# Kernel optimization log

Measured on AMD Instinct MI355X. Metric: run time of the kernel, lower is better.

The kernel has to match this reference:

```python
import jax, jax.numpy as jnp
import numpy as np

N_HEADS = 4
DIM_K = 64
DIM_V = 64
D_MODEL = 256


def setup_inputs() -> dict:
    key = jax.random.key(0)
    ks = jax.random.split(key, 10)
    B, S = 8, 1024
    s = 1.0 / np.sqrt(D_MODEL)
    return {
        "x": jax.random.normal(ks[0], (B, S, D_MODEL), jnp.float32),
        "y": jax.random.normal(ks[1], (B, S, D_MODEL), jnp.float32),
        "Wq": jax.random.normal(ks[2], (D_MODEL, DIM_K * N_HEADS), jnp.float32) * s,
        "bq": jnp.zeros((DIM_K * N_HEADS,), jnp.float32),
        "Wk": jax.random.normal(ks[3], (D_MODEL, DIM_K * N_HEADS), jnp.float32) * s,
        "bk": jnp.zeros((DIM_K * N_HEADS,), jnp.float32),
        "Wv": jax.random.normal(ks[4], (D_MODEL, DIM_V * N_HEADS), jnp.float32) * s,
        "bv": jnp.zeros((DIM_V * N_HEADS,), jnp.float32),
        "Wo": jax.random.normal(ks[5], (DIM_V * N_HEADS, D_MODEL), jnp.float32) * s,
        "bo": jnp.zeros((D_MODEL,), jnp.float32),
    }


def reference(x, y, Wq, bq, Wk, bk, Wv, bv, Wo, bo):
    B, Sx, _ = x.shape
    Sy = y.shape[1]
    dk = DIM_K // N_HEADS  # head dim for Q/K (16)
    dv = DIM_V // N_HEADS  # head dim for V (16)
    # Faithful to the original reshape: leading dim becomes n_heads^2 pseudo-heads.
    Q = (x @ Wq + bq).reshape(-1, B, Sx, dk)   # [H2, B, Sx, dk]
    K = (y @ Wk + bk).reshape(-1, B, Sy, dk)   # [H2, B, Sy, dk]
    V = (y @ Wv + bv).reshape(-1, B, Sy, dv)   # [H2, B, Sy, dv]
    scale = 1.0 / np.sqrt(DIM_K)
    scores = jnp.einsum("hbqd,hbkd->hbqk", Q, K) * scale  # [H2, B, Sx, Sy]
    # Per-row lower median (torch.median semantics: lower of two middle values).
    n = scores.shape[-1]
    med = jnp.sort(scores, axis=-1)[..., (n - 1) // 2][..., None]
    # Mask out entries not strictly greater than the row median.
    scores = jnp.where(scores - med > 0, scores, -jnp.inf)
    probs = jax.nn.softmax(scores, axis=-1)
    out = jnp.einsum("hbqk,hbkd->hbqd", probs, V)          # [H2, B, Sx, dv]
    out = jnp.transpose(out, (0, 2, 1, 3)).reshape(B, Sx, -1)  # [B, Sx, H2*dv]
    return out @ Wo + bo
```

## Files before the change

### kernel.cpp

```cpp
#include <hip/hip_runtime.h>
#include <stdint.h>


typedef _Float16 f16x8 __attribute__((ext_vector_type(8)));
typedef _Float16 f16x4 __attribute__((ext_vector_type(4)));
typedef float    f32x4 __attribute__((ext_vector_type(4)));

__global__ __launch_bounds__(256) void prepW(
    const float* __restrict__ Wq, const float* __restrict__ Wk,
    const float* __restrict__ Wv, const float* __restrict__ Wo,
    _Float16* __restrict__ P)
{
    __shared__ float T[64][65];
    const int mat = blockIdx.y;
    const float* W = (mat == 0) ? Wq : (mat == 1) ? Wk : (mat == 2) ? Wv : Wo;
    const int tk = blockIdx.x >> 2, tn = blockIdx.x & 3;
    const int t  = threadIdx.x;
    const int cl = t & 63, rg = t >> 6;

    #pragma unroll
    for (int r = 0; r < 16; ++r) {
        const int k = (rg << 4) + r;
        T[k][cl] = W[(size_t)((tk << 6) + k) * 256 + (tn << 6) + cl];
    }
    __syncthreads();
    _Float16* hi = P + ((size_t)mat << 17);
    _Float16* lo = hi + 65536;
    #pragma unroll
    for (int r = 0; r < 16; ++r) {
        const int n = (rg << 4) + r;
        const float v = T[cl][n];
        const _Float16 h = (_Float16)v;
        const size_t o = (size_t)((tn << 6) + n) * 256 + (tk << 6) + cl;
        hi[o] = h;
        lo[o] = (_Float16)(v - (float)h);
    }
}

__device__ __forceinline__ void gemm_mfma(const float* __restrict__ A,
                                          const _Float16* __restrict__ Whi,
                                          const _Float16* __restrict__ Wlo,
                                          const float* __restrict__ bias,
                                          float* __restrict__ C, int vf16)
{
    __shared__ _Float16 Bhi[64][136];
    __shared__ _Float16 Blo[64][136];
    const int tid = threadIdx.x;
    const int m0 = blockIdx.x << 7, n0 = blockIdx.y << 6;

    const int wv = tid >> 6, lane = tid & 63;
    const int fm = lane & 15, fq = lane >> 4;
    const int arow = m0 + (wv << 4) + fm;
    const float* abase = A + (size_t)arow * 256;

    const int srow = tid >> 4;
    const int skl  = (tid & 15) << 3;

    f32x4 acc[4];
    #pragma unroll
    for (int cb = 0; cb < 4; ++cb) { acc[cb][0]=0.f; acc[cb][1]=0.f; acc[cb][2]=0.f; acc[cb][3]=0.f; }

    float4 a0 = *(const float4*)(abase + (fq << 3));
    float4 a1 = *(const float4*)(abase + (fq << 3) + 4);

    #pragma unroll
    for (int h = 0; h < 2; ++h) {
        if (h) __syncthreads();
        #pragma unroll
        for (int p = 0; p < 2; ++p) {
            const int n = (p << 5) + srow;
            const size_t off = (size_t)(n0 + n) * 256 + (h << 7) + skl;
            *(f16x8*)&Bhi[n][skl] = *(const f16x8*)(Whi + off);
            *(f16x8*)&Blo[n][skl] = *(const f16x8*)(Wlo + off);
        }
        __syncthreads();

        #pragma unroll
        for (int kb = 0; kb < 4; ++kb) {
            const int ks = (h << 2) + kb;
            float4 n0v = a0, n1v = a1;
            if (ks < 7) {
                const float* np = abase + ((ks + 1) << 5) + (fq << 3);
                n0v = *(const float4*)np;
                n1v = *(const float4*)(np + 4);
            }
            const float ae[8] = {a0.x, a0.y, a0.z, a0.w, a1.x, a1.y, a1.z, a1.w};
            f16x8 Ah, Al;
            #pragma unroll
            for (int j = 0; j < 8; ++j) {
                const _Float16 hh = (_Float16)ae[j];
                Ah[j] = hh;
                Al[j] = (_Float16)(ae[j] - (float)hh);
            }
            #pragma unroll
            for (int cb = 0; cb < 4; ++cb) {
                f16x8 Bh = *(const f16x8*)&Bhi[(cb << 4) + fm][(kb << 5) + (fq << 3)];
                f16x8 Bl = *(const f16x8*)&Blo[(cb << 4) + fm][(kb << 5) + (fq << 3)];
                acc[cb] = __builtin_amdgcn_mfma_f32_16x16x32_f16(Ah, Bh, acc[cb], 0, 0, 0);
                acc[cb] = __builtin_amdgcn_mfma_f32_16x16x32_f16(Al, Bh, acc[cb], 0, 0, 0);
                acc[cb] = __builtin_amdgcn_mfma_f32_16x16x32_f16(Ah, Bl, acc[cb], 0, 0, 0);
            }
            a0 = n0v; a1 = n1v;
        }
    }

    if (vf16) {
        _Float16* Vt = (_Float16*)C;
        float bb[4];
        #pragma unroll
        for (int cb = 0; cb < 4; ++cb) bb[cb] = bias[n0 + (cb << 4) + fm];
        #pragma unroll
        for (int i = 0; i < 4; ++i) {
            const int m = m0 + (wv << 4) + (fq << 2) + i;
            f16x4 v;
            #pragma unroll
            for (int cb = 0; cb < 4; ++cb)
                v[cb] = (_Float16)(acc[cb][i] + bb[cb]);
            const size_t o = ((size_t)(m >> 6) << 14) + ((size_t)fm << 10)
                           + ((m & 63) << 4) + (n0 >> 4);
            *(f16x4*)&Vt[o] = v;
        }
    } else {
        #pragma unroll
        for (int cb = 0; cb < 4; ++cb) {
            const float bb = bias[n0 + (cb << 4) + fm];
            #pragma unroll
            for (int i = 0; i < 4; ++i)
                C[(size_t)(m0 + (wv << 4) + (fq << 2) + i) * 256
                  + n0 + (cb << 4) + fm] = acc[cb][i] + bb;
        }
    }
}

__global__ __attribute__((amdgpu_waves_per_eu(6, 6)))
__launch_bounds__(512) void gemmQKV(
    const float* __restrict__ x, const float* __restrict__ y,
    const _Float16* __restrict__ WP,
    const float* __restrict__ bq, const float* __restrict__ bk,
    const float* __restrict__ bv,
    float* __restrict__ Q, float* __restrict__ K, float* __restrict__ Vf)
{
    const int z = blockIdx.z;
    const float* A = (z == 0) ? x  : y;
    const _Float16* Whi = WP + ((size_t)z << 17);
    const _Float16* Wlo = Whi + 65536;
    const float* b = (z == 0) ? bq : (z == 1) ? bk : bv;
    float*       C = (z == 0) ? Q  : (z == 1) ? K  : Vf;
    gemm_mfma(A, Whi, Wlo, b, C, z == 2);
}

__global__ __attribute__((amdgpu_waves_per_eu(6, 6)))
__launch_bounds__(512) void gemmOut(
    const float* __restrict__ A, const _Float16* __restrict__ WP,
    const float* __restrict__ b, float* __restrict__ C)
{
    const _Float16* Whi = WP + ((size_t)3 << 17);
    const _Float16* Wlo = Whi + 65536;
    gemm_mfma(A, Whi, Wlo, b, C, 0);
}

__device__ __forceinline__ float u2f(unsigned int m) {
    unsigned int x = (m & 0x80000000u) ? (m ^ 0x80000000u) : ~m;
    return __uint_as_float(x);
}
__device__ __forceinline__ unsigned int f2u(float f) {
    unsigned int x = __float_as_uint(f);
    return (x & 0x80000000u) ? ~x : (x | 0x80000000u);
}

__device__ __forceinline__ float wred_sum(float x) {
    x += __int_as_float(__builtin_amdgcn_update_dpp(0, __float_as_int(x), 0x111, 0xF, 0xF, true));
    x += __int_as_float(__builtin_amdgcn_update_dpp(0, __float_as_int(x), 0x112, 0xF, 0xF, true));
    x += __int_as_float(__builtin_amdgcn_update_dpp(0, __float_as_int(x), 0x114, 0xF, 0xF, true));
    x += __int_as_float(__builtin_amdgcn_update_dpp(0, __float_as_int(x), 0x118, 0xF, 0xF, true));
    x += __int_as_float(__builtin_amdgcn_update_dpp(0, __float_as_int(x), 0x142, 0xF, 0xF, true));
    x += __int_as_float(__builtin_amdgcn_update_dpp(0, __float_as_int(x), 0x143, 0xF, 0xF, true));
    return __int_as_float(__builtin_amdgcn_readlane(__float_as_int(x), 63));
}
__device__ __forceinline__ float wred_min(float x) {
    const int IDENT = 0x7f7fffff;
    x = fminf(x, __int_as_float(__builtin_amdgcn_update_dpp(IDENT, __float_as_int(x), 0x111, 0xF, 0xF, false)));
    x = fminf(x, __int_as_float(__builtin_amdgcn_update_dpp(IDENT, __float_as_int(x), 0x112, 0xF, 0xF, false)));
    x = fminf(x, __int_as_float(__builtin_amdgcn_update_dpp(IDENT, __float_as_int(x), 0x114, 0xF, 0xF, false)));
    x = fminf(x, __int_as_float(__builtin_amdgcn_update_dpp(IDENT, __float_as_int(x), 0x118, 0xF, 0xF, false)));
    x = fminf(x, __int_as_float(__builtin_amdgcn_update_dpp(IDENT, __float_as_int(x), 0x142, 0xF, 0xF, false)));
    x = fminf(x, __int_as_float(__builtin_amdgcn_update_dpp(IDENT, __float_as_int(x), 0x143, 0xF, 0xF, false)));
    return __int_as_float(__builtin_amdgcn_readlane(__float_as_int(x), 63));
}
__device__ __forceinline__ float wred_max(float x) {
    const int IDENT = (int)0xff7fffff;
    x = fmaxf(x, __int_as_float(__builtin_amdgcn_update_dpp(IDENT, __float_as_int(x), 0x111, 0xF, 0xF, false)));
    x = fmaxf(x, __int_as_float(__builtin_amdgcn_update_dpp(IDENT, __float_as_int(x), 0x112, 0xF, 0xF, false)));
    x = fmaxf(x, __int_as_float(__builtin_amdgcn_update_dpp(IDENT, __float_as_int(x), 0x114, 0xF, 0xF, false)));
    x = fmaxf(x, __int_as_float(__builtin_amdgcn_update_dpp(IDENT, __float_as_int(x), 0x118, 0xF, 0xF, false)));
    x = fmaxf(x, __int_as_float(__builtin_amdgcn_update_dpp(IDENT, __float_as_int(x), 0x142, 0xF, 0xF, false)));
    x = fmaxf(x, __int_as_float(__builtin_amdgcn_update_dpp(IDENT, __float_as_int(x), 0x143, 0xF, 0xF, false)));
    return __int_as_float(__builtin_amdgcn_readlane(__float_as_int(x), 63));
}

__global__ __attribute__((amdgpu_waves_per_eu(6, 6)))
__launch_bounds__(512) void attn(
    const float* __restrict__ Qb, const float* __restrict__ Kb,
    const _Float16* __restrict__ Vb, float* __restrict__ Ob)
{
    __shared__ float Ssc[8][1028];
    __shared__ float part[1024];
    __shared__ float sums[2][8];

    const int tid  = threadIdx.x;
    const int wave = tid >> 6, lane = tid & 63;
    const int head = blockIdx.x, grp = blockIdx.y;
    const float*    Qh = Qb + ((size_t)head << 14);
    const float*    Kh = Kb + ((size_t)head << 14);
    const _Float16* Vh = Vb + ((size_t)head << 14);
    const int fm = lane & 15, fq = lane >> 4;

    f16x8 Bp[8];
    #pragma unroll
    for (int kb = 0; kb < 8; ++kb) {
        const int krow = (wave << 7) + (kb << 4) + fm;
        float4 kv = *(const float4*)(Kh + ((size_t)krow << 4) + (fq << 2));
        const float ke[4] = {kv.x * 0.125f, kv.y * 0.125f,
                             kv.z * 0.125f, kv.w * 0.125f};
        #pragma unroll
        for (int j = 0; j < 4; ++j) {
            _Float16 h = (_Float16)ke[j];
            Bp[kb][j]     = h;
            Bp[kb][j + 4] = (_Float16)(ke[j] - (float)h);
        }
    }
    const _Float16* vfb = Vh + ((size_t)fm << 10) + (wave << 7) + (fq << 3);

    const int cstart = (grp * 128) / 6;
    const int cend   = ((grp + 1) * 128) / 6;

    for (int chunk = cstart; chunk < cend; ++chunk) {
        const int qbase = chunk << 3;
        const int sb = chunk & 1;

        f16x8 A1, A2;
        {
            const int arow = qbase + (fm & 7);
            float4 qv = *(const float4*)(Qh + ((size_t)arow << 4) + (fq << 2));
            const float qe[4] = {qv.x, qv.y, qv.z, qv.w};
            #pragma unroll
            for (int j = 0; j < 4; ++j) {
                _Float16 h = (_Float16)qe[j];
                A1[j] = h; A1[j + 4] = h;
                A2[j] = (_Float16)(qe[j] - (float)h);
                A2[j + 4] = (_Float16)0.f;
            }
        }
        #pragma unroll
        for (int kb = 0; kb < 8; ++kb) {
            f32x4 c = {0.f, 0.f, 0.f, 0.f};
            c = __builtin_amdgcn_mfma_f32_16x16x32_f16(A1, Bp[kb], c, 0, 0, 0);
            c = __builtin_amdgcn_mfma_f32_16x16x32_f16(A2, Bp[kb], c, 0, 0, 0);
            if (fq < 2) {
                const int col = (wave << 7) + (kb << 4) + fm;
                #pragma unroll
                for (int i = 0; i < 4; ++i)
                    Ssc[(fq << 2) + i][col] = c[i];
            }
        }
        __syncthreads();

        float s[16];
        #pragma unroll
        for (int b = 0; b < 4; ++b) {
            f32x4 v = *(const f32x4*)&Ssc[wave][(b << 8) + (lane << 2)];
            s[(b << 2) + 0] = v.x; s[(b << 2) + 1] = v.y;
            s[(b << 2) + 2] = v.z; s[(b << 2) + 3] = v.w;
        }

        float mn = 0.f, sq = 0.f;
        #pragma unroll
        for (int j = 0; j < 16; ++j) { mn += s[j]; sq += s[j] * s[j]; }
        mn = wred_sum(mn);
        sq = wred_sum(sq);
        mn *= (1.0f / 1024.0f);
        const float var  = fmaxf(sq * (1.0f / 1024.0f) - mn * mn, 1e-12f);
        const float step = __builtin_sqrtf(var) * 0.0024479f;

        unsigned int lo = 0x00800000u, hi = 0xFF7FFFFFu;
        int cl = 0, ch = 1024;
        float vL = -3.4e38f, vH = 3.4e38f;
        float t = mn, medf = 0.f;
        int found = 0;
        for (int pass = 0; pass < 64 && !found; ++pass) {
            int cnt = 0;
            #pragma unroll
            for (int j = 0; j < 16; ++j)
                cnt += __popcll(__ballot(s[j] <= t));
            const unsigned int tc = f2u(t);
            if (cnt >= 512) { hi = tc; ch = cnt; vH = t; }
            else            { lo = tc + 1; cl = cnt; vL = t; }

            if (cl == 511) {
                float c = 3.4e38f;
                #pragma unroll
                for (int j = 0; j < 16; ++j)
                    c = fminf(c, (s[j] > vL) ? s[j] : 3.4e38f);
                medf = wred_min(c); found = 1;
            } else if (ch == 512) {
                float c = -3.4e38f;
                #pragma unroll
                for (int j = 0; j < 16; ++j)
                    c = fmaxf(c, (s[j] <= vH) ? s[j] : -3.4e38f);
                medf = wred_max(c); found = 1;
            } else if (cl == 510) {
                float m1 = 3.4e38f;
                #pragma unroll
                for (int j = 0; j < 16; ++j)
                    m1 = fminf(m1, (s[j] > vL) ? s[j] : 3.4e38f);
                m1 = wred_min(m1);
                int c1 = 0;
                #pragma unroll
                for (int j = 0; j < 16; ++j)
                    c1 += __popcll(__ballot(s[j] <= m1));
                if (c1 >= 512) { medf = m1; }
                else {
                    float c2 = 3.4e38f;
                    #pragma unroll
                    for (int j = 0; j < 16; ++j)
                        c2 = fminf(c2, (s[j] > m1) ? s[j] : 3.4e38f);
                    medf = wred_min(c2);
                }
                found = 1;
            } else if (ch == 513) {
                float m1 = -3.4e38f;
                #pragma unroll
                for (int j = 0; j < 16; ++j)
                    m1 = fmaxf(m1, (s[j] <= vH) ? s[j] : -3.4e38f);
                m1 = wred_max(m1);
                int c1 = 0;
                #pragma unroll
                for (int j = 0; j < 16; ++j)
                    c1 += __popcll(__ballot(s[j] < m1));
                if (c1 <= 511) { medf = m1; }
                else {
                    float c2 = -3.4e38f;
                    #pragma unroll
                    for (int j = 0; j < 16; ++j)
                        c2 = fmaxf(c2, (s[j] < m1) ? s[j] : -3.4e38f);
                    medf = wred_max(c2);
                }
                found = 1;
            } else if (lo >= hi) {
                medf = u2f(lo); found = 1;
            } else {
                float tn = t + (511.5f - (float)cnt) * step;
                bool ok = (tn > vL) && (tn < vH);
                if (pass >= 5 && (pass & 1)) ok = false;
                t = ok ? tn : u2f(lo + ((hi - lo) >> 1));
            }
        }
        if (!found) medf = u2f(lo);

        _Float16* Pw = (_Float16*)&Ssc[wave][0];
        float sum = 0.f;
        #pragma unroll
        for (int b = 0; b < 4; ++b) {
            f16x4 hv;
            #pragma unroll
            for (int jj = 0; jj < 4; ++jj) {
                float e = (s[(b << 2) + jj] > medf) ? __expf(s[(b << 2) + jj]) : 0.f;
                _Float16 h = (_Float16)e;
                hv[jj] = h;
                sum += (float)h;
            }
            *(f16x4*)&Pw[(b << 8) + (lane << 2)] = hv;
        }
        sum = wred_sum(sum);
        if (lane == 0) sums[sb][wave] = sum;
        __syncthreads();

        f32x4 acc = {0.f, 0.f, 0.f, 0.f};
        const _Float16* Pr = (const _Float16*)&Ssc[fm & 7][0] + (fq << 3);
        #pragma unroll
        for (int kb = 0; kb < 4; ++kb) {
            f16x8 vf = *(const f16x8*)(vfb + (kb << 5));
            f16x8 a = *(const f16x8*)(Pr + ((((wave << 2) + kb)) << 5));
            acc = __builtin_amdgcn_mfma_f32_16x16x32_f16(a, vf, acc, 0, 0, 0);
        }
        if (lane < 32) {
            #pragma unroll
            for (int i = 0; i < 4; ++i)
                part[(wave << 7) + (((fq << 2) + i) << 4) + fm] = acc[i];
        }
        __syncthreads();

        const int rw = (wave - chunk) & 7;
        if (rw < 2) {
            const int t2 = (rw << 6) + lane;
            const int r = t2 >> 4, d = t2 & 15;
            float o = 0.f;
            #pragma unroll
            for (int w = 0; w < 8; ++w) o += part[(w << 7) + t2];
            const float inv = 1.0f / sums[sb][r];
            const int q = qbase + r;
            const int h = head >> 3, bp = head & 7;
            float* dst = Ob + (((size_t)(h >> 1)) << 18)
                            + ((size_t)(((h & 1) << 9) + (q >> 1)) << 8)
                            + ((q & 1) << 7) + (bp << 4) + d;
            *dst = o * inv;
        }
    }
}

extern "C" void kernel_launch(void* const* d_in, const int* in_sizes, int n_in,
                              void* d_out, int out_size, void* d_ws, size_t ws_size,
                              hipStream_t stream) {
    const float* x  = (const float*)d_in[0];
    const float* y  = (const float*)d_in[1];
    const float* Wq = (const float*)d_in[2];
    const float* bq = (const float*)d_in[3];
    const float* Wk = (const float*)d_in[4];
    const float* bk = (const float*)d_in[5];
    const float* Wv = (const float*)d_in[6];
    const float* bv = (const float*)d_in[7];
    const float* Wo = (const float*)d_in[8];
    const float* bo = (const float*)d_in[9];
    float* out = (float*)d_out;

    float*     Q  = (float*)d_ws;
    float*     K  = Q + 2097152;
    _Float16*  VT = (_Float16*)(K + 2097152);
    float*     AO = (float*)d_ws + 5242880;
    _Float16*  WP = (_Float16*)((float*)d_ws + 7340032);

    prepW<<<dim3(16, 4), dim3(256), 0, stream>>>(Wq, Wk, Wv, Wo, WP);
    gemmQKV<<<dim3(64, 4, 3), dim3(512), 0, stream>>>(x, y, WP, bq, bk, bv,
                                                      Q, K, (float*)VT);
    attn<<<dim3(128, 6), dim3(512), 0, stream>>>(Q, K, VT, AO);
    gemmOut<<<dim3(64, 4), dim3(512), 0, stream>>>(AO, WP, bo, out);
}
```

Measured before the change: 260.4 us.

## Pre-swizzle weights into MFMA fragment layout and read directly from global

prepW now writes the hi/lo fp16 weight split in the exact per-lane MFMA B-fragment order, so the GEMM kernels load B fragments straight from global memory with 16-byte loads. This removes the LDS staging and both __syncthreads in the GEMM. Blocks shrink to 256 threads covering 64 rows, and the grids double to keep the same coverage. The cost is redundant B reads from global/L2 across blocks and one fewer wave of latency hiding per block.

```diff
diff --git a/kernel.cpp b/kernel.cpp
--- a/kernel.cpp
+++ b/kernel.cpp
@@ -27,13 +27,23 @@
     _Float16* hi = P + ((size_t)mat << 17);
     _Float16* lo = hi + 65536;
     #pragma unroll
-    for (int r = 0; r < 16; ++r) {
-        const int n = (rg << 4) + r;
-        const float v = T[cl][n];
-        const _Float16 h = (_Float16)v;
-        const size_t o = (size_t)((tn << 6) + n) * 256 + (tk << 6) + cl;
-        hi[o] = h;
-        lo[o] = (_Float16)(v - (float)h);
+    for (int ff = 0; ff < 2; ++ff) {
+        const int f    = (ff << 8) + t;
+        const int lane = f & 63, cb = (f >> 6) & 3, kbl = f >> 8;
+        const int fm = lane & 15, fq = lane >> 4;
+        const int kb = (tk << 1) + kbl;
+        const size_t dst = ((size_t)tn << 14) + ((size_t)((kb << 2) + cb) << 9)
+                         + ((size_t)lane << 3);
+        f16x8 vh, vl;
+        #pragma unroll
+        for (int j = 0; j < 8; ++j) {
+            const float v = T[(kbl << 5) + (fq << 3) + j][(cb << 4) + fm];
+            const _Float16 h = (_Float16)v;
+            vh[j] = h;
+            vl[j] = (_Float16)(v - (float)h);
+        }
+        *(f16x8*)&hi[dst] = vh;
+        *(f16x8*)&lo[dst] = vl;
     }
 }
 
@@ -43,18 +53,15 @@
                                           const float* __restrict__ bias,
                                           float* __restrict__ C, int vf16)
 {
-    __shared__ _Float16 Bhi[64][136];
-    __shared__ _Float16 Blo[64][136];
     const int tid = threadIdx.x;
-    const int m0 = blockIdx.x << 7, n0 = blockIdx.y << 6;
+    const int m0 = blockIdx.x << 6, n0 = blockIdx.y << 6;
 
     const int wv = tid >> 6, lane = tid & 63;
     const int fm = lane & 15, fq = lane >> 4;
     const int arow = m0 + (wv << 4) + fm;
     const float* abase = A + (size_t)arow * 256;
-
-    const int srow = tid >> 4;
-    const int skl  = (tid & 15) << 3;
+    const _Float16* bhF = Whi + ((size_t)blockIdx.y << 14) + ((size_t)lane << 3);
+    const _Float16* blF = Wlo + ((size_t)blockIdx.y << 14) + ((size_t)lane << 3);
 
     f32x4 acc[4];
     #pragma unroll
@@ -64,44 +71,31 @@
     float4 a1 = *(const float4*)(abase + (fq << 3) + 4);
 
     #pragma unroll
-    for (int h = 0; h < 2; ++h) {
-        if (h) __syncthreads();
-        #pragma unroll
-        for (int p = 0; p < 2; ++p) {
-            const int n = (p << 5) + srow;
-            const size_t off = (size_t)(n0 + n) * 256 + (h << 7) + skl;
-            *(f16x8*)&Bhi[n][skl] = *(const f16x8*)(Whi + off);
-            *(f16x8*)&Blo[n][skl] = *(const f16x8*)(Wlo + off);
-        }
-        __syncthreads();
-
-        #pragma unroll
-        for (int kb = 0; kb < 4; ++kb) {
-            const int ks = (h << 2) + kb;
-            float4 n0v = a0, n1v = a1;
-            if (ks < 7) {
-                const float* np = abase + ((ks + 1) << 5) + (fq << 3);
-                n0v = *(const float4*)np;
-                n1v = *(const float4*)(np + 4);
-            }
-            const float ae[8] = {a0.x, a0.y, a0.z, a0.w, a1.x, a1.y, a1.z, a1.w};
-            f16x8 Ah, Al;
-            #pragma unroll
-            for (int j = 0; j < 8; ++j) {
-                const _Float16 hh = (_Float16)ae[j];
-                Ah[j] = hh;
-                Al[j] = (_Float16)(ae[j] - (float)hh);
-            }
-            #pragma unroll
-            for (int cb = 0; cb < 4; ++cb) {
-                f16x8 Bh = *(const f16x8*)&Bhi[(cb << 4) + fm][(kb << 5) + (fq << 3)];
-                f16x8 Bl = *(const f16x8*)&Blo[(cb << 4) + fm][(kb << 5) + (fq << 3)];
-                acc[cb] = __builtin_amdgcn_mfma_f32_16x16x32_f16(Ah, Bh, acc[cb], 0, 0, 0);
-                acc[cb] = __builtin_amdgcn_mfma_f32_16x16x32_f16(Al, Bh, acc[cb], 0, 0, 0);
-                acc[cb] = __builtin_amdgcn_mfma_f32_16x16x32_f16(Ah, Bl, acc[cb], 0, 0, 0);
-            }
-            a0 = n0v; a1 = n1v;
-        }
+    for (int ks = 0; ks < 8; ++ks) {
+        float4 n0v = a0, n1v = a1;
+        if (ks < 7) {
+            const float* np = abase + ((ks + 1) << 5) + (fq << 3);
+            n0v = *(const float4*)np;
+            n1v = *(const float4*)(np + 4);
+        }
+        const float ae[8] = {a0.x, a0.y, a0.z, a0.w, a1.x, a1.y, a1.z, a1.w};
+        f16x8 Ah, Al;
+        #pragma unroll
+        for (int j = 0; j < 8; ++j) {
+            const _Float16 hh = (_Float16)ae[j];
+            Ah[j] = hh;
+            Al[j] = (_Float16)(ae[j] - (float)hh);
+        }
+        #pragma unroll
+        for (int cb = 0; cb < 4; ++cb) {
+            const size_t off = (size_t)(((ks << 2) + cb) << 9);
+            f16x8 Bh = *(const f16x8*)(bhF + off);
+            f16x8 Bl = *(const f16x8*)(blF + off);
+            acc[cb] = __builtin_amdgcn_mfma_f32_16x16x32_f16(Ah, Bh, acc[cb], 0, 0, 0);
+            acc[cb] = __builtin_amdgcn_mfma_f32_16x16x32_f16(Al, Bh, acc[cb], 0, 0, 0);
+            acc[cb] = __builtin_amdgcn_mfma_f32_16x16x32_f16(Ah, Bl, acc[cb], 0, 0, 0);
+        }
+        a0 = n0v; a1 = n1v;
     }
 
     if (vf16) {
@@ -132,8 +126,8 @@
     }
 }
 
-__global__ __attribute__((amdgpu_waves_per_eu(6, 6)))
-__launch_bounds__(512) void gemmQKV(
+__global__ __attribute__((amdgpu_waves_per_eu(4, 4)))
+__launch_bounds__(256) void gemmQKV(
     const float* __restrict__ x, const float* __restrict__ y,
     const _Float16* __restrict__ WP,
     const float* __restrict__ bq, const float* __restrict__ bk,
@@ -149,8 +143,8 @@
     gemm_mfma(A, Whi, Wlo, b, C, z == 2);
 }
 
-__global__ __attribute__((amdgpu_waves_per_eu(6, 6)))
-__launch_bounds__(512) void gemmOut(
+__global__ __attribute__((amdgpu_waves_per_eu(4, 4)))
+__launch_bounds__(256) void gemmOut(
     const float* __restrict__ A, const _Float16* __restrict__ WP,
     const float* __restrict__ b, float* __restrict__ C)
 {
@@ -430,8 +424,8 @@
     _Float16*  WP = (_Float16*)((float*)d_ws + 7340032);
 
     prepW<<<dim3(16, 4), dim3(256), 0, stream>>>(Wq, Wk, Wv, Wo, WP);
-    gemmQKV<<<dim3(64, 4, 3), dim3(512), 0, stream>>>(x, y, WP, bq, bk, bv,
-                                                      Q, K, (float*)VT);
+    gemmQKV<<<dim3(128, 4, 3), dim3(256), 0, stream>>>(x, y, WP, bq, bk, bv,
+                                                       Q, K, (float*)VT);
     attn<<<dim3(128, 6), dim3(512), 0, stream>>>(Q, K, VT, AO);
-    gemmOut<<<dim3(64, 4), dim3(512), 0, stream>>>(AO, WP, bo, out);
-}
+    gemmOut<<<dim3(128, 4), dim3(256), 0, stream>>>(AO, WP, bo, out);
+}
```

Measured after the change: 271.7 us. 4.4% more time.

## Defer output reduction into next iteration to drop one barrier per chunk

Applied to the files above, without the earlier changes.

Gives the fp16 probabilities their own shared-memory buffer (Pbuf) so they no longer overwrite the score buffer. The cross-wave reduction of partial PV results for chunk c-1 can then run after the barrier that follows chunk c's score computation, removing one __syncthreads per loop iteration. A final epilogue after the loop handles the last chunk. Shared memory per block grows by about 16 KB, which may lower occupancy.

```diff
diff --git a/kernel.cpp b/kernel.cpp
--- a/kernel.cpp
+++ b/kernel.cpp
@@ -203,9 +203,10 @@
     const float* __restrict__ Qb, const float* __restrict__ Kb,
     const _Float16* __restrict__ Vb, float* __restrict__ Ob)
 {
-    __shared__ float Ssc[8][1028];
-    __shared__ float part[1024];
-    __shared__ float sums[2][8];
+    __shared__ float    Ssc[8][1028];
+    __shared__ _Float16 Pbuf[8][1032];
+    __shared__ float    part[1024];
+    __shared__ float    sums[2][8];
 
     const int tid  = threadIdx.x;
     const int wave = tid >> 6, lane = tid & 63;
@@ -264,6 +265,25 @@
             }
         }
         __syncthreads();
+
+        if (chunk > cstart) {
+            const int pc = chunk - 1;
+            const int rw = (wave - pc) & 7;
+            if (rw < 2) {
+                const int t2 = (rw << 6) + lane;
+                const int r = t2 >> 4, d = t2 & 15;
+                float o = 0.f;
+                #pragma unroll
+                for (int w = 0; w < 8; ++w) o += part[(w << 7) + t2];
+                const float inv = 1.0f / sums[pc & 1][r];
+                const int q = (pc << 3) + r;
+                const int h = head >> 3, bp = head & 7;
+                float* dst = Ob + (((size_t)(h >> 1)) << 18)
+                                + ((size_t)(((h & 1) << 9) + (q >> 1)) << 8)
+                                + ((q & 1) << 7) + (bp << 4) + d;
+                *dst = o * inv;
+            }
+        }
 
         float s[16];
         #pragma unroll
@@ -357,7 +377,7 @@
         }
         if (!found) medf = u2f(lo);
 
-        _Float16* Pw = (_Float16*)&Ssc[wave][0];
+        _Float16* Pw = &Pbuf[wave][0];
         float sum = 0.f;
         #pragma unroll
         for (int b = 0; b < 4; ++b) {
@@ -376,7 +396,7 @@
         __syncthreads();
 
         f32x4 acc = {0.f, 0.f, 0.f, 0.f};
-        const _Float16* Pr = (const _Float16*)&Ssc[fm & 7][0] + (fq << 3);
+        const _Float16* Pr = &Pbuf[fm & 7][0] + (fq << 3);
         #pragma unroll
         for (int kb = 0; kb < 4; ++kb) {
             f16x8 vf = *(const f16x8*)(vfb + (kb << 5));
@@ -388,17 +408,20 @@
             for (int i = 0; i < 4; ++i)
                 part[(wave << 7) + (((fq << 2) + i) << 4) + fm] = acc[i];
         }
-        __syncthreads();
-
-        const int rw = (wave - chunk) & 7;
+    }
+
+    __syncthreads();
+    {
+        const int pc = cend - 1;
+        const int rw = (wave - pc) & 7;
         if (rw < 2) {
             const int t2 = (rw << 6) + lane;
             const int r = t2 >> 4, d = t2 & 15;
             float o = 0.f;
             #pragma unroll
             for (int w = 0; w < 8; ++w) o += part[(w << 7) + t2];
-            const float inv = 1.0f / sums[sb][r];
-            const int q = qbase + r;
+            const float inv = 1.0f / sums[pc & 1][r];
+            const int q = (pc << 3) + r;
             const int h = head >> 3, bp = head & 7;
             float* dst = Ob + (((size_t)(h >> 1)) << 18)
                             + ((size_t)(((h & 1) << 9) + (q >> 1)) << 8)
```

After: 260.6 us. About the same (+0.1%).
